# Optimization experiments

Hardware: AMD Instinct MI355X
Metric: run time of the kernel (lower is better)

The kernel has to match this reference:

```python
import jax, jax.numpy as jnp
import numpy as np
from jax import lax

D_MODEL = 1024
D_IN = 1024        # expand=1 -> d_inner = d_model
N_STATE = 16       # d_state
DT_RANK = 64       # ceil(d_model/16)
D_FFN = 4096
BATCH, SEQ = 2, 2048


def setup_inputs() -> dict:
    key = jax.random.key(0)
    ks = jax.random.split(key, 12)
    r = lambda i, shape, s=0.02: jax.random.normal(ks[i], shape, jnp.float32) * s
    ones = lambda n: jnp.ones((n,), jnp.float32)
    zeros = lambda n: jnp.zeros((n,), jnp.float32)
    # S4D-real init for A
    A_log = jnp.log(jnp.tile(jnp.arange(1, N_STATE + 1, dtype=jnp.float32), (D_IN, 1)))
    return {
        "src": jax.random.normal(ks[0], (BATCH, SEQ, D_MODEL), jnp.float32),
        "in_proj_w": r(1, (2 * D_IN, D_MODEL)),
        "conv_w": r(2, (D_IN, 2), 0.5),
        "conv_b": zeros(D_IN),
        "x_proj_w": r(3, (DT_RANK + 2 * N_STATE, D_IN)),
        "dt_proj_w": r(4, (D_IN, DT_RANK), 0.1),
        "dt_proj_b": r(5, (D_IN,), 0.1),
        "A_log": A_log,
        "Dp": ones(D_IN),
        "out_proj_w": r(6, (D_MODEL, D_IN)),
        "mnorm_g": ones(D_MODEL), "mnorm_b": zeros(D_MODEL),
        "n1_g": ones(D_MODEL), "n1_b": zeros(D_MODEL),
        "n2_g": ones(D_MODEL), "n2_b": zeros(D_MODEL),
        "n3_g": ones(D_MODEL), "n3_b": zeros(D_MODEL),
        "ffn_w1": r(7, (D_FFN, D_MODEL)),
        "ffn_w2": r(8, (D_MODEL, D_FFN)),
        "fe_w": r(9, (D_MODEL, D_MODEL)),
        "fe_b": zeros(D_MODEL),
    }


def _ln(x, g, b, eps=1e-5):
    m = x.mean(-1, keepdims=True)
    v = ((x - m) ** 2).mean(-1, keepdims=True)
    return (x - m) / jnp.sqrt(v + eps) * g + b


def _mamba(x, in_proj_w, conv_w, conv_b, x_proj_w, dt_proj_w, dt_proj_b,
           A_log, Dp, out_proj_w):
    B, L, _ = x.shape
    xz = x @ in_proj_w.T                       # (B,L,2*D_IN)
    x_in, z = jnp.split(xz, 2, axis=-1)
    # depthwise causal conv1d, kernel size 2: y[l] = w0*x[l-1] + w1*x[l] + b
    x_prev = jnp.pad(x_in, ((0, 0), (1, 0), (0, 0)))[:, :L]
    x_c = jax.nn.silu(x_prev * conv_w[:, 0] + x_in * conv_w[:, 1] + conv_b)
    x_dbl = x_c @ x_proj_w.T                   # (B,L,DT_RANK+2N)
    dt, Bm, Cm = jnp.split(x_dbl, [DT_RANK, DT_RANK + N_STATE], axis=-1)
    delta = jax.nn.softplus(dt @ dt_proj_w.T + dt_proj_b)   # (B,L,D_IN)
    A = -jnp.exp(A_log)                        # (D_IN,N)
    deltaA = jnp.exp(delta[..., None] * A)                   # (B,L,D_IN,N)
    dBu = delta[..., None] * Bm[:, :, None, :] * x_c[..., None]

    def step(h, t):
        dA_t, dBu_t, C_t = t                   # (B,D_IN,N),(B,D_IN,N),(B,N)
        h = dA_t * h + dBu_t
        y = jnp.einsum('bdn,bn->bd', h, C_t)
        return h, y

    h0 = jnp.zeros((B, D_IN, N_STATE), x.dtype)
    _, ys = lax.scan(step, h0,
                     (deltaA.transpose(1, 0, 2, 3),
                      dBu.transpose(1, 0, 2, 3),
                      Cm.transpose(1, 0, 2)))
    y = ys.transpose(1, 0, 2)                  # (B,L,D_IN)
    y = (y + x_c * Dp) * jax.nn.silu(z)
    return y @ out_proj_w.T


def reference(src, in_proj_w, conv_w, conv_b, x_proj_w, dt_proj_w, dt_proj_b,
              A_log, Dp, out_proj_w, mnorm_g, mnorm_b, n1_g, n1_b, n2_g, n2_b,
              n3_g, n3_b, ffn_w1, ffn_w2, fe_w, fe_b):
    # src1 = MambaBlock(norm1(src)); dropout = identity (eval)
    h = _mamba(_ln(src, n1_g, n1_b), in_proj_w, conv_w, conv_b, x_proj_w,
               dt_proj_w, dt_proj_b, A_log, Dp, out_proj_w)
    src = src + _ln(h, mnorm_g, mnorm_b)
    # FFN: Linear -> LeakyReLU(0.01) -> Linear (no bias)
    f = _ln(src, n2_g, n2_b) @ ffn_w1.T
    f = jnp.where(f >= 0, f, 0.01 * f) @ ffn_w2.T
    src = src + f
    src = src + (_ln(src, n3_g, n3_b) @ fe_w.T + fe_b)
    return src
```

## Files before the change

### kernel.cpp

```cpp
#include <hip/hip_runtime.h>
#include <hip/hip_bf16.h>
#include <cstddef>

#define L_SEQ   2048
#define NBATCH  2
#define NROWS   (NBATCH * L_SEQ)
#define NSTATE  16
#define CH      64
#define NCHUNK  (L_SEQ / CH)

typedef __bf16 bf16x8 __attribute__((ext_vector_type(8)));
typedef float  f32x4  __attribute__((ext_vector_type(4)));
typedef unsigned short u16x4 __attribute__((ext_vector_type(4)));
typedef unsigned short u16x8 __attribute__((ext_vector_type(8)));

static __device__ __forceinline__ unsigned short f2bf(float f) {
  unsigned int x = __builtin_bit_cast(unsigned int, f);
  x += 0x7fffu + ((x >> 16) & 1u);
  return (unsigned short)(x >> 16);
}
static __device__ __forceinline__ float bf2f(unsigned short u) {
  return __builtin_bit_cast(float, ((unsigned int)u) << 16);
}

#define GLDS(g, l) __builtin_amdgcn_global_load_lds( \
    (const __attribute__((address_space(1))) void*)(g), \
    (__attribute__((address_space(3))) void*)(l), 16, 0, 0)

#define DRAIN_VM() asm volatile("s_waitcnt vmcnt(0)" ::: "memory")

__global__ __launch_bounds__(256) void cvt_bf16_kernel(
    const float* __restrict__ in, unsigned short* __restrict__ out, int n4)
{
  const int i = blockIdx.x * 256 + threadIdx.x;
  if (i < n4) {
    const float4 v = reinterpret_cast<const float4*>(in)[i];
    u16x4 o;
    o[0] = f2bf(v.x); o[1] = f2bf(v.y); o[2] = f2bf(v.z); o[3] = f2bf(v.w);
    reinterpret_cast<u16x4*>(out)[i] = o;
  }
}

__global__ __launch_bounds__(256) void cvt_all_kernel(
    const float* __restrict__ ipw, const float* __restrict__ xpw,
    const float* __restrict__ dtw, const float* __restrict__ opw,
    const float* __restrict__ w1,  const float* __restrict__ w2,
    const float* __restrict__ few, float* __restrict__ zx,
    unsigned short* __restrict__ o_ipw, unsigned short* __restrict__ o_xpw,
    unsigned short* __restrict__ o_dtw, unsigned short* __restrict__ o_opw,
    unsigned short* __restrict__ o_w1,  unsigned short* __restrict__ o_w2,
    unsigned short* __restrict__ o_few,
    const float* __restrict__ lsrc, const float* __restrict__ lg,
    const float* __restrict__ lb, unsigned short* __restrict__ louth)
{
  __shared__ float sm[8];
  if (blockIdx.x >= 12832) {
    const int row = blockIdx.x - 12832;
    const int tid = threadIdx.x;
    const float4 v = reinterpret_cast<const float4*>(lsrc + (size_t)row * 1024)[tid];
    float s = v.x + v.y + v.z + v.w;
#pragma unroll
    for (int o = 32; o > 0; o >>= 1) s += __shfl_down(s, o, 64);
    if ((tid & 63) == 0) sm[tid >> 6] = s;
    __syncthreads();
    const float mean = (sm[0] + sm[1] + sm[2] + sm[3]) * (1.f / 1024.f);
    const float dx = v.x - mean, dy = v.y - mean, dz = v.z - mean, dw = v.w - mean;
    float q = dx * dx + dy * dy + dz * dz + dw * dw;
#pragma unroll
    for (int o = 32; o > 0; o >>= 1) q += __shfl_down(q, o, 64);
    __syncthreads();
    if ((tid & 63) == 0) sm[tid >> 6] = q;
    __syncthreads();
    const float var = (sm[0] + sm[1] + sm[2] + sm[3]) * (1.f / 1024.f);
    const float rstd = rsqrtf(var + 1e-5f);
    const float4 gv = reinterpret_cast<const float4*>(lg)[tid];
    const float4 bv = reinterpret_cast<const float4*>(lb)[tid];
    u16x4 ob;
    ob[0] = f2bf(dx * rstd * gv.x + bv.x);
    ob[1] = f2bf(dy * rstd * gv.y + bv.y);
    ob[2] = f2bf(dz * rstd * gv.z + bv.z);
    ob[3] = f2bf(dw * rstd * gv.w + bv.w);
    reinterpret_cast<u16x4*>(louth + (size_t)row * 1024)[tid] = ob;
    return;
  }
  int i = blockIdx.x * 256 + threadIdx.x;
  if (i < 98304) {
    reinterpret_cast<float4*>(zx)[i] = make_float4(0.f, 0.f, 0.f, 0.f);
    return;
  }
  i -= 98304;
  const float* src; unsigned short* dst;
  if (i < 524288)                 { src = ipw; dst = o_ipw; }
  else if ((i -= 524288) < 24576) { src = xpw; dst = o_xpw; }
  else if ((i -= 24576) < 16384)  { src = dtw; dst = o_dtw; }
  else if ((i -= 16384) < 262144) { src = opw; dst = o_opw; }
  else if ((i -= 262144) < 1048576){ src = w1; dst = o_w1; }
  else if ((i -= 1048576) < 1048576){ src = w2; dst = o_w2; }
  else if ((i -= 1048576) < 262144){ src = few; dst = o_few; }
  else return;
  const float4 v = reinterpret_cast<const float4*>(src)[i];
  u16x4 o;
  o[0] = f2bf(v.x); o[1] = f2bf(v.y); o[2] = f2bf(v.z); o[3] = f2bf(v.w);
  reinterpret_cast<u16x4*>(dst)[i] = o;
}

__global__ __launch_bounds__(256) void ln_kernel(
    const float* __restrict__ in, const float* __restrict__ g,
    const float* __restrict__ bta, const float* __restrict__ res,
    float* __restrict__ out, unsigned short* __restrict__ outb)
{
  const int row = blockIdx.x;
  const int tid = threadIdx.x;
  __shared__ float sm[8];
  const float4 v = reinterpret_cast<const float4*>(in + (size_t)row * 1024)[tid];
  float s = v.x + v.y + v.z + v.w;
#pragma unroll
  for (int o = 32; o > 0; o >>= 1) s += __shfl_down(s, o, 64);
  if ((tid & 63) == 0) sm[tid >> 6] = s;
  __syncthreads();
  const float mean = (sm[0] + sm[1] + sm[2] + sm[3]) * (1.f / 1024.f);
  const float dx = v.x - mean, dy = v.y - mean, dz = v.z - mean, dw = v.w - mean;
  float q = dx * dx + dy * dy + dz * dz + dw * dw;
#pragma unroll
  for (int o = 32; o > 0; o >>= 1) q += __shfl_down(q, o, 64);
  __syncthreads();
  if ((tid & 63) == 0) sm[tid >> 6] = q;
  __syncthreads();
  const float var = (sm[0] + sm[1] + sm[2] + sm[3]) * (1.f / 1024.f);
  const float rstd = rsqrtf(var + 1e-5f);
  const float4 gv = reinterpret_cast<const float4*>(g)[tid];
  const float4 bv = reinterpret_cast<const float4*>(bta)[tid];
  float4 o4;
  o4.x = dx * rstd * gv.x + bv.x;
  o4.y = dy * rstd * gv.y + bv.y;
  o4.z = dz * rstd * gv.z + bv.z;
  o4.w = dw * rstd * gv.w + bv.w;
  if (outb) {
    u16x4 ob;
    ob[0] = f2bf(o4.x); ob[1] = f2bf(o4.y); ob[2] = f2bf(o4.z); ob[3] = f2bf(o4.w);
    reinterpret_cast<u16x4*>(outb + (size_t)row * 1024)[tid] = ob;
  } else {
    if (res) {
      const float4 rv = reinterpret_cast<const float4*>(res + (size_t)row * 1024)[tid];
      o4.x += rv.x; o4.y += rv.y; o4.z += rv.z; o4.w += rv.w;
    }
    reinterpret_cast<float4*>(out + (size_t)row * 1024)[tid] = o4;
  }
}

__global__ __launch_bounds__(256) void ln2_kernel(
    const float* __restrict__ in, const float* __restrict__ g1,
    const float* __restrict__ b1, const float* __restrict__ res,
    const float* __restrict__ g2, const float* __restrict__ b2,
    float* __restrict__ out1, unsigned short* __restrict__ out2b)
{
  const int row = blockIdx.x;
  const int tid = threadIdx.x;
  __shared__ float sm[8];
  const float4 v = reinterpret_cast<const float4*>(in + (size_t)row * 1024)[tid];
  float s = v.x + v.y + v.z + v.w;
#pragma unroll
  for (int o = 32; o > 0; o >>= 1) s += __shfl_down(s, o, 64);
  if ((tid & 63) == 0) sm[tid >> 6] = s;
  __syncthreads();
  const float mean = (sm[0] + sm[1] + sm[2] + sm[3]) * (1.f / 1024.f);
  const float dx = v.x - mean, dy = v.y - mean, dz = v.z - mean, dw = v.w - mean;
  float q = dx * dx + dy * dy + dz * dz + dw * dw;
#pragma unroll
  for (int o = 32; o > 0; o >>= 1) q += __shfl_down(q, o, 64);
  __syncthreads();
  if ((tid & 63) == 0) sm[tid >> 6] = q;
  __syncthreads();
  const float var = (sm[0] + sm[1] + sm[2] + sm[3]) * (1.f / 1024.f);
  const float rstd = rsqrtf(var + 1e-5f);
  const float4 g1v = reinterpret_cast<const float4*>(g1)[tid];
  const float4 b1v = reinterpret_cast<const float4*>(b1)[tid];
  const float4 rv = reinterpret_cast<const float4*>(res + (size_t)row * 1024)[tid];
  float4 o4;
  o4.x = dx * rstd * g1v.x + b1v.x + rv.x;
  o4.y = dy * rstd * g1v.y + b1v.y + rv.y;
  o4.z = dz * rstd * g1v.z + b1v.z + rv.z;
  o4.w = dw * rstd * g1v.w + b1v.w + rv.w;
  reinterpret_cast<float4*>(out1 + (size_t)row * 1024)[tid] = o4;
  __syncthreads();
  float s2 = o4.x + o4.y + o4.z + o4.w;
#pragma unroll
  for (int o = 32; o > 0; o >>= 1) s2 += __shfl_down(s2, o, 64);
  if ((tid & 63) == 0) sm[tid >> 6] = s2;
  __syncthreads();
  const float mean2 = (sm[0] + sm[1] + sm[2] + sm[3]) * (1.f / 1024.f);
  const float ex = o4.x - mean2, ey = o4.y - mean2, ez = o4.z - mean2, ew = o4.w - mean2;
  float q2 = ex * ex + ey * ey + ez * ez + ew * ew;
#pragma unroll
  for (int o = 32; o > 0; o >>= 1) q2 += __shfl_down(q2, o, 64);
  __syncthreads();
  if ((tid & 63) == 0) sm[tid >> 6] = q2;
  __syncthreads();
  const float var2 = (sm[0] + sm[1] + sm[2] + sm[3]) * (1.f / 1024.f);
  const float rstd2 = rsqrtf(var2 + 1e-5f);
  const float4 g2v = reinterpret_cast<const float4*>(g2)[tid];
  const float4 b2v = reinterpret_cast<const float4*>(b2)[tid];
  u16x4 ob;
  ob[0] = f2bf(ex * rstd2 * g2v.x + b2v.x);
  ob[1] = f2bf(ey * rstd2 * g2v.y + b2v.y);
  ob[2] = f2bf(ez * rstd2 * g2v.z + b2v.z);
  ob[3] = f2bf(ew * rstd2 * g2v.w + b2v.w);
  reinterpret_cast<u16x4*>(out2b + (size_t)row * 1024)[tid] = ob;
}

__global__ __launch_bounds__(512) void gemm256_kernel(
    const unsigned short* __restrict__ A, int lda,
    const unsigned short* __restrict__ B, int ldb,
    void* __restrict__ Cv, int ldc,
    const float* __restrict__ bias, const float* __restrict__ res,
    int K, int act, int outbf, int gy)
{
  __shared__ __align__(16) unsigned char smem[131072];
  const int t = threadIdx.x;
  const int w = t >> 6, l = t & 63;

  const int q = gridDim.x >> 3;
  const int nid = (blockIdx.x & 7) * q + (blockIdx.x >> 3);
  const int bm = (nid / gy) * 256;
  const int bn = (nid % gy) * 256;

  const int wr = (w >> 2) * 128;
  const int wc = (w & 3) * 64;
  f32x4 acc[8][4] = {};

  const int srow = t >> 2;
  const int sk = (t & 3) * 8;
  const unsigned short* gA = A + (size_t)(bm + srow) * lda + sk;
  const unsigned short* gB = B + (size_t)(bn + srow) * ldb + sk;

  const int fr = l & 15;
  const int kb = (l >> 4) * 8;

#define SA7(s) (smem + (s) * 16384)
#define SB7(s) (smem + 65536 + (s) * 16384)

#define STAGE7(s, k0) do { \
    GLDS(gA + (k0), SA7(s) + w * 1024); \
    GLDS(gA + (k0) + (size_t)128 * lda, SA7(s) + 8192 + w * 1024); \
    GLDS(gB + (k0), SB7(s) + w * 1024); \
    GLDS(gB + (k0) + (size_t)128 * ldb, SB7(s) + 8192 + w * 1024); \
  } while (0)

#define COMPUTE7(s) do { \
    bf16x8 af[8], bfr[4]; \
    _Pragma("unroll") \
    for (int j = 0; j < 4; ++j) \
      bfr[j] = *reinterpret_cast<const bf16x8*>((const unsigned short*)SB7(s) + (wc + j * 16 + fr) * 32 + kb); \
    _Pragma("unroll") \
    for (int i = 0; i < 8; ++i) \
      af[i] = *reinterpret_cast<const bf16x8*>((const unsigned short*)SA7(s) + (wr + i * 16 + fr) * 32 + kb); \
    _Pragma("unroll") \
    for (int i = 0; i < 8; ++i) \
      _Pragma("unroll") \
      for (int j = 0; j < 4; ++j) \
        acc[i][j] = __builtin_amdgcn_mfma_f32_16x16x32_bf16(af[i], bfr[j], acc[i][j], 0, 0, 0); \
  } while (0)

  const int nt = K >> 5;
  STAGE7(0, 0);
  if (nt > 1) STAGE7(1, 32);
  if (nt > 2) STAGE7(2, 64);
  if (nt > 2)      asm volatile("s_waitcnt vmcnt(8)" ::: "memory");
  else if (nt > 1) asm volatile("s_waitcnt vmcnt(4)" ::: "memory");
  else             asm volatile("s_waitcnt vmcnt(0)" ::: "memory");
  __builtin_amdgcn_s_barrier();
  for (int kt = 0; kt < nt; ++kt) {
    const int s = kt & 3;
    __builtin_amdgcn_sched_barrier(0);
    if (kt + 3 < nt) STAGE7((kt + 3) & 3, (kt + 3) * 32);
    __builtin_amdgcn_sched_barrier(0);
    COMPUTE7(s);
    __builtin_amdgcn_sched_barrier(0);
    if (kt + 3 < nt)      asm volatile("s_waitcnt vmcnt(8)" ::: "memory");
    else if (kt + 2 < nt) asm volatile("s_waitcnt vmcnt(4)" ::: "memory");
    else if (kt + 1 < nt) asm volatile("s_waitcnt vmcnt(0)" ::: "memory");
    __builtin_amdgcn_s_barrier();
  }
#undef STAGE7
#undef COMPUTE7
#undef SA7
#undef SB7

  const int crow = (l >> 4) * 4;
  const int ccol = l & 15;
  float* Cf = (float*)Cv;
  unsigned short* Cb = (unsigned short*)Cv;
#pragma unroll
  for (int i = 0; i < 8; ++i) {
#pragma unroll
    for (int j = 0; j < 4; ++j) {
      const int n = bn + wc + j * 16 + ccol;
      const float bv = bias ? bias[n] : 0.f;
#pragma unroll
      for (int r = 0; r < 4; ++r) {
        const int m = bm + wr + i * 16 + crow + r;
        float v = acc[i][j][r] + bv;
        if (act == 1) v = (v > 20.f) ? v : __logf(1.f + __expf(v));
        else if (act == 2) v = (v >= 0.f) ? v : 0.01f * v;
        if (res) v += res[(size_t)m * ldc + n];
        if (outbf) Cb[(size_t)m * ldc + n] = f2bf(v);
        else       Cf[(size_t)m * ldc + n] = v;
      }
    }
  }
}

template<int BK>
__global__ __launch_bounds__(512) void gemm_ksplit_kernel(
    const unsigned short* __restrict__ A, int lda,
    const unsigned short* __restrict__ B, int ldb,
    void* __restrict__ Cv, int ldc,
    const float* __restrict__ bias, const float* __restrict__ res,
    int K, int act, int outbf, int gy)
{
  constexpr int ABYTES = 128 * BK * 2;
  constexpr int NISS = (BK == 32) ? 2 : 4;
  constexpr int RPI  = (BK == 32) ? 64 : 32;
  constexpr int NS   = BK / 32;
  __shared__ __align__(16) unsigned char smem[8 * ABYTES];
  const int tid = threadIdx.x;
  const int grp = tid >> 8;
  const int t = tid & 255;
  const int w = t >> 6, l = t & 63;

  const int q = gridDim.x >> 3;
  const int nid = (blockIdx.x & 7) * q + (blockIdx.x >> 3);
  const int bm = (nid / gy) * 128;
  const int bn = (nid % gy) * 128;

  const int K2 = K >> 1;
  const int koff = grp * K2;
  const int wr = (w >> 1) * 64, wc = (w & 1) * 64;
  f32x4 acc[4][4] = {};

  const int srow = (BK == 32) ? (t >> 2) : (t >> 3);
  const int sk   = (BK == 32) ? ((t & 3) * 8) : ((t & 7) * 8);
  const unsigned short* gA = A + (size_t)(bm + srow) * lda + koff + sk;
  const unsigned short* gB = B + (size_t)(bn + srow) * ldb + koff + sk;

  const int gbase = grp * 2 * ABYTES;
  const int fr = l & 15;
  const int kb = (l >> 4) * 8;

#define SAb(buf) (smem + gbase + (buf) * ABYTES)
#define SBb(buf) (smem + 4 * ABYTES + gbase + (buf) * ABYTES)

#define STAGEK(buf, k0) do { \
    _Pragma("unroll") \
    for (int ii = 0; ii < NISS; ++ii) { \
      GLDS(gA + (k0) + (size_t)ii * RPI * lda, SAb(buf) + ii * 4096 + w * 1024); \
      GLDS(gB + (k0) + (size_t)ii * RPI * ldb, SBb(buf) + ii * 4096 + w * 1024); \
    } \
  } while (0)

#define COMPUTEK(buf) do { \
    _Pragma("unroll") \
    for (int s = 0; s < NS; ++s) { \
      bf16x8 af[4], bfr[4]; \
      _Pragma("unroll") \
      for (int i = 0; i < 4; ++i) \
        af[i] = *reinterpret_cast<const bf16x8*>((const unsigned short*)SAb(buf) + (wr + i * 16 + fr) * BK + s * 32 + kb); \
      _Pragma("unroll") \
      for (int j = 0; j < 4; ++j) \
        bfr[j] = *reinterpret_cast<const bf16x8*>((const unsigned short*)SBb(buf) + (wc + j * 16 + fr) * BK + s * 32 + kb); \
      _Pragma("unroll") \
      for (int i = 0; i < 4; ++i) \
        _Pragma("unroll") \
        for (int j = 0; j < 4; ++j) \
          acc[i][j] = __builtin_amdgcn_mfma_f32_16x16x32_bf16(af[i], bfr[j], acc[i][j], 0, 0, 0); \
    } \
  } while (0)

  STAGEK(0, 0);
  DRAIN_VM();
  __syncthreads();
  int cur = 0;
  for (int k0 = BK; k0 < K2; k0 += BK) {
    __builtin_amdgcn_sched_barrier(0);
    STAGEK(cur ^ 1, k0);
    __builtin_amdgcn_sched_barrier(0);
    COMPUTEK(cur);
    DRAIN_VM();
    __syncthreads();
    cur ^= 1;
  }
  COMPUTEK(cur);
#undef STAGEK
#undef COMPUTEK
#undef SAb
#undef SBb

  __syncthreads();
  float* red = (float*)smem;
  if (grp) {
#pragma unroll
    for (int i = 0; i < 4; ++i)
#pragma unroll
      for (int j = 0; j < 4; ++j)
        *reinterpret_cast<f32x4*>(&red[(t << 6) + (i * 4 + j) * 4]) = acc[i][j];
  }
  __syncthreads();
  if (!grp) {
    const int crow = (l >> 4) * 4;
    const int ccol = l & 15;
    float* Cf = (float*)Cv;
    unsigned short* Cb = (unsigned short*)Cv;
#pragma unroll
    for (int i = 0; i < 4; ++i) {
#pragma unroll
      for (int j = 0; j < 4; ++j) {
        const f32x4 o = *reinterpret_cast<const f32x4*>(&red[(t << 6) + (i * 4 + j) * 4]);
        const int n = bn + wc + j * 16 + ccol;
        const float bv = bias ? bias[n] : 0.f;
#pragma unroll
        for (int r = 0; r < 4; ++r) {
          const int m = bm + wr + i * 16 + crow + r;
          float v = acc[i][j][r] + o[r] + bv;
          if (act == 1) v = (v > 20.f) ? v : __logf(1.f + __expf(v));
          else if (act == 2) v = (v >= 0.f) ? v : 0.01f * v;
          if (res) v += res[(size_t)m * ldc + n];
          if (outbf) Cb[(size_t)m * ldc + n] = f2bf(v);
          else       Cf[(size_t)m * ldc + n] = v;
        }
      }
    }
  }
}

__global__ __launch_bounds__(256) void xproj_kernel(
    const unsigned short* __restrict__ A, int lda,
    const unsigned short* __restrict__ B, int ldb,
    float* __restrict__ C)
{
  __shared__ unsigned short As[2][128 * 32];
  __shared__ unsigned short Bs[2][96 * 32];
  const int t = threadIdx.x;
  const int w = t >> 6, l = t & 63;
  const int bm = blockIdx.x * 128;
  const int kbase = blockIdx.y * 128;

  f32x4 acc[2][6] = {};

  const int srow = t >> 2;
  const int sk = (t & 3) * 8;
  const unsigned short* gA0 = A + (size_t)(bm + srow) * lda + kbase + sk;
  const unsigned short* gA1 = gA0 + (size_t)64 * lda;
  const unsigned short* gB0 = B + (size_t)srow * ldb + kbase + sk;
  const unsigned short* gB1 = gB0 + (size_t)64 * ldb;

  const int fr = l & 15;
  const int kb = (l >> 4) * 8;

#define STAGEX(buf, k0) do { \
    GLDS(gA0 + (k0), &As[buf][w * 512]); \
    GLDS(gA1 + (k0), &As[buf][2048 + w * 512]); \
    GLDS(gB0 + (k0), &Bs[buf][w * 512]); \
    if (w < 2) GLDS(gB1 + (k0), &Bs[buf][2048 + w * 512]); \
  } while (0)

#define COMPUTEX(buf) do { \
    bf16x8 af[2], bfr[6]; \
    _Pragma("unroll") \
    for (int i = 0; i < 2; ++i) \
      af[i] = *reinterpret_cast<const bf16x8*>(&As[buf][(w * 32 + i * 16 + fr) * 32 + kb]); \
    _Pragma("unroll") \
    for (int j = 0; j < 6; ++j) \
      bfr[j] = *reinterpret_cast<const bf16x8*>(&Bs[buf][(j * 16 + fr) * 32 + kb]); \
    _Pragma("unroll") \
    for (int i = 0; i < 2; ++i) \
      _Pragma("unroll") \
      for (int j = 0; j < 6; ++j) \
        acc[i][j] = __builtin_amdgcn_mfma_f32_16x16x32_bf16(af[i], bfr[j], acc[i][j], 0, 0, 0); \
  } while (0)

  STAGEX(0, 0);
  DRAIN_VM();
  __syncthreads();
  int cur = 0;
  for (int s = 1; s < 4; ++s) {
    __builtin_amdgcn_sched_barrier(0);
    STAGEX(cur ^ 1, s * 32);
    __builtin_amdgcn_sched_barrier(0);
    COMPUTEX(cur);
    DRAIN_VM();
    __syncthreads();
    cur ^= 1;
  }
  COMPUTEX(cur);
#undef STAGEX
#undef COMPUTEX

  const int crow = (l >> 4) * 4;
  const int ccol = l & 15;
#pragma unroll
  for (int i = 0; i < 2; ++i)
#pragma unroll
    for (int j = 0; j < 6; ++j)
#pragma unroll
      for (int r = 0; r < 4; ++r) {
        const int m = bm + w * 32 + i * 16 + crow + r;
        const int n = j * 16 + ccol;
        atomicAdd(&C[(size_t)m * 96 + n], acc[i][j][r]);
      }
}

__global__ __launch_bounds__(256) void conv_silu_kernel(
    const unsigned short* __restrict__ xz, const float* __restrict__ cw,
    const float* __restrict__ cb, unsigned short* __restrict__ xcb)
{
  const int i = blockIdx.x * 256 + threadIdx.x;
  const int row = i >> 7;
  const int dv = (i & 127) * 8;
  const int l = row & (L_SEQ - 1);
  const u16x8 cur = *reinterpret_cast<const u16x8*>(&xz[(size_t)row * 2048 + dv]);
  u16x8 prev = {};
  if (l != 0) prev = *reinterpret_cast<const u16x8*>(&xz[(size_t)(row - 1) * 2048 + dv]);
  float cwv[16], cbv[8];
#pragma unroll
  for (int qq = 0; qq < 4; ++qq)
    *reinterpret_cast<float4*>(&cwv[qq * 4]) = reinterpret_cast<const float4*>(cw + 2 * dv)[qq];
#pragma unroll
  for (int qq = 0; qq < 2; ++qq)
    *reinterpret_cast<float4*>(&cbv[qq * 4]) = reinterpret_cast<const float4*>(cb + dv)[qq];
  u16x8 o;
#pragma unroll
  for (int e = 0; e < 8; ++e) {
    const float v = bf2f(prev[e]) * cwv[2 * e] + bf2f(cur[e]) * cwv[2 * e + 1] + cbv[e];
    o[e] = f2bf(v / (1.f + __expf(-v)));
  }
  *reinterpret_cast<u16x8*>(&xcb[(size_t)row * 1024 + dv]) = o;
}

__global__ __launch_bounds__(256) void scan_pass1(
    const unsigned short* __restrict__ delta, const unsigned short* __restrict__ xc,
    const float* __restrict__ xdbl, const float* __restrict__ A_log,
    unsigned short* __restrict__ hfin, unsigned short* __restrict__ pcum)
{
  const int tid = threadIdx.x;
  const int db = blockIdx.x & 3;
  const int c = (blockIdx.x >> 2) & (NCHUNK - 1);
  const int b = blockIdx.x >> 7;
  const int d = db * 256 + tid;
  __shared__ float Bsh[CH][16];
  {
    const int lr = tid >> 2, q = tid & 3;
    const float* p = xdbl + ((size_t)(b * L_SEQ + c * CH + lr) * 96) + 64 + q * 4;
    *reinterpret_cast<float4*>(&Bsh[lr][q * 4]) = *reinterpret_cast<const float4*>(p);
  }
  float a[NSTATE];
#pragma unroll
  for (int n = 0; n < NSTATE; ++n) a[n] = -__expf(A_log[d * 16 + n]);
  __syncthreads();
  float h[NSTATE], P[NSTATE];
#pragma unroll
  for (int n = 0; n < NSTATE; ++n) { h[n] = 0.f; P[n] = 1.f; }
  const size_t rowbase = (size_t)(b * L_SEQ + c * CH);
  for (int s = 0; s < CH; ++s) {
    const size_t row = rowbase + s;
    const float dl = bf2f(delta[row * 1024 + d]);
    const float xcv = bf2f(xc[row * 1024 + d]);
#pragma unroll
    for (int n = 0; n < NSTATE; ++n) {
      const float dA = __expf(dl * a[n]);
      h[n] = h[n] * dA + (dl * Bsh[s][n]) * xcv;
      P[n] *= dA;
    }
  }
  const size_t base = ((size_t)((b * NCHUNK + c) * 1024 + d)) * 16;
  u16x8 h0, h1, p0, p1;
#pragma unroll
  for (int n = 0; n < 8; ++n) {
    h0[n] = f2bf(h[n]);     h1[n] = f2bf(h[n + 8]);
    p0[n] = f2bf(P[n]);     p1[n] = f2bf(P[n + 8]);
  }
  *reinterpret_cast<u16x8*>(hfin + base) = h0;
  *reinterpret_cast<u16x8*>(hfin + base + 8) = h1;
  *reinterpret_cast<u16x8*>(pcum + base) = p0;
  *reinterpret_cast<u16x8*>(pcum + base + 8) = p1;
}

__global__ __launch_bounds__(256) void scan_pass2(
    const unsigned short* __restrict__ hfin, const unsigned short* __restrict__ pcum,
    unsigned short* __restrict__ hstart)
{
  const int t = blockIdx.x * 256 + threadIdx.x;
  const int b = t >> 14;
  const int dn = t & 16383;
  const size_t base = (size_t)b * NCHUNK * 16384 + dn;
  float h = 0.f;
  for (int c = 0; c < NCHUNK; ++c) {
    const size_t idx = base + (size_t)c * 16384;
    hstart[idx] = f2bf(h);
    h = bf2f(pcum[idx]) * h + bf2f(hfin[idx]);
  }
}

__global__ __launch_bounds__(256) void scan_pass3(
    const unsigned short* __restrict__ delta, const unsigned short* __restrict__ xc,
    const float* __restrict__ xdbl, const float* __restrict__ A_log,
    const unsigned short* __restrict__ hstart, const float* __restrict__ Dp,
    const unsigned short* __restrict__ xz, unsigned short* __restrict__ yout)
{
  const int tid = threadIdx.x;
  const int db = blockIdx.x & 3;
  const int c = (blockIdx.x >> 2) & (NCHUNK - 1);
  const int b = blockIdx.x >> 7;
  const int d = db * 256 + tid;
  __shared__ float Bsh[CH][16];
  __shared__ float Csh[CH][16];
  {
    const int lr = tid >> 2, q = tid & 3;
    const float* p = xdbl + ((size_t)(b * L_SEQ + c * CH + lr) * 96);
    *reinterpret_cast<float4*>(&Bsh[lr][q * 4]) = *reinterpret_cast<const float4*>(p + 64 + q * 4);
    *reinterpret_cast<float4*>(&Csh[lr][q * 4]) = *reinterpret_cast<const float4*>(p + 80 + q * 4);
  }
  float a[NSTATE];
#pragma unroll
  for (int n = 0; n < NSTATE; ++n) a[n] = -__expf(A_log[d * 16 + n]);
  float h[NSTATE];
  {
    const size_t base = ((size_t)((b * NCHUNK + c) * 1024 + d)) * 16;
    const u16x8 v0 = *reinterpret_cast<const u16x8*>(hstart + base);
    const u16x8 v1 = *reinterpret_cast<const u16x8*>(hstart + base + 8);
#pragma unroll
    for (int n = 0; n < 8; ++n) { h[n] = bf2f(v0[n]); h[n + 8] = bf2f(v1[n]); }
  }
  const float dpv = Dp[d];
  __syncthreads();
  const size_t rowbase = (size_t)(b * L_SEQ + c * CH);
  for (int s = 0; s < CH; ++s) {
    const size_t row = rowbase + s;
    const float dl = bf2f(delta[row * 1024 + d]);
    const float xcv = bf2f(xc[row * 1024 + d]);
    float y = 0.f;
#pragma unroll
    for (int n = 0; n < NSTATE; ++n) {
      const float dA = __expf(dl * a[n]);
      h[n] = h[n] * dA + (dl * Bsh[s][n]) * xcv;
      y += h[n] * Csh[s][n];
    }
    const float z = bf2f(xz[row * 2048 + 1024 + d]);
    const float sil = z / (1.f + __expf(-z));
    yout[row * 1024 + d] = f2bf((y + xcv * dpv) * sil);
  }
}

extern "C" void kernel_launch(void* const* d_in, const int* in_sizes, int n_in,
                              void* d_out, int out_size, void* d_ws, size_t ws_size,
                              hipStream_t stream)
{
  (void)in_sizes; (void)n_in; (void)out_size; (void)ws_size;
  const float* src        = (const float*)d_in[0];
  const float* in_proj_w  = (const float*)d_in[1];
  const float* conv_w     = (const float*)d_in[2];
  const float* conv_b     = (const float*)d_in[3];
  const float* x_proj_w   = (const float*)d_in[4];
  const float* dt_proj_w  = (const float*)d_in[5];
  const float* dt_proj_b  = (const float*)d_in[6];
  const float* A_log      = (const float*)d_in[7];
  const float* Dp         = (const float*)d_in[8];
  const float* out_proj_w = (const float*)d_in[9];
  const float* mnorm_g    = (const float*)d_in[10];
  const float* mnorm_b    = (const float*)d_in[11];
  const float* n1_g       = (const float*)d_in[12];
  const float* n1_b       = (const float*)d_in[13];
  const float* n2_g       = (const float*)d_in[14];
  const float* n2_b       = (const float*)d_in[15];
  const float* n3_g       = (const float*)d_in[16];
  const float* n3_b       = (const float*)d_in[17];
  const float* ffn_w1     = (const float*)d_in[18];
  const float* ffn_w2     = (const float*)d_in[19];
  const float* fe_w       = (const float*)d_in[20];
  const float* fe_b       = (const float*)d_in[21];
  float* out = (float*)d_out;
  float* ws  = (float*)d_ws;

  unsigned short* xzb   = (unsigned short*)ws;
  unsigned short* xdblb = (unsigned short*)(ws + 4194304);
  unsigned short* dtwb  = (unsigned short*)(ws + 4390912);
  unsigned short* deltab= (unsigned short*)(ws + 4423680);
  float* xdbl  = ws + 12582912;
  float* s5    = ws + 17301504;
  float* src1  = ws + 21495808;
  unsigned short* hfin = (unsigned short*)(ws + 25690112);
  unsigned short* pcum = (unsigned short*)(ws + 26738688);
  unsigned short* hst  = (unsigned short*)(ws + 27787264);
  unsigned short* s1b  = (unsigned short*)(ws + 28835840);
  unsigned short* xcb  = (unsigned short*)(ws + 30932992);
  unsigned short* yb   = (unsigned short*)(ws + 33030144);
  unsigned short* f1b  = (unsigned short*)(ws + 35127296);
  unsigned short* ipwb = (unsigned short*)(ws + 43515904);
  unsigned short* xpwb = (unsigned short*)(ws + 44564480);
  unsigned short* opwb = (unsigned short*)(ws + 44613632);
  unsigned short* w1b  = (unsigned short*)(ws + 45137920);
  unsigned short* w2b  = (unsigned short*)(ws + 47235072);
  unsigned short* fewb = (unsigned short*)(ws + 49332224);

  const dim3 blk(256);
  const dim3 blk512(512);

  cvt_all_kernel<<<16928, blk, 0, stream>>>(
      in_proj_w, x_proj_w, dt_proj_w, out_proj_w, ffn_w1, ffn_w2, fe_w, xdbl,
      ipwb, xpwb, dtwb, opwb, w1b, w2b, fewb,
      src, n1_g, n1_b, s1b);

  gemm_ksplit_kernel<32><<<512, blk512, 0, stream>>>(s1b, 1024, ipwb, 1024, xzb, 2048,
                                                     nullptr, nullptr, 1024, 0, 1, 16);
  conv_silu_kernel<<<2048, blk, 0, stream>>>(xzb, conv_w, conv_b, xcb);
  xproj_kernel<<<dim3(32, 8), blk, 0, stream>>>(xcb, 1024, xpwb, 1024, xdbl);
  cvt_bf16_kernel<<<384, blk, 0, stream>>>(xdbl, xdblb, 98304);
  gemm_ksplit_kernel<32><<<256, blk512, 0, stream>>>(xdblb, 96, dtwb, 64, deltab, 1024,
                                                     dt_proj_b, nullptr, 64, 1, 1, 8);
  scan_pass1<<<256, blk, 0, stream>>>(deltab, xcb, xdbl, A_log, hfin, pcum);
  scan_pass2<<<128, blk, 0, stream>>>(hfin, pcum, hst);
  scan_pass3<<<256, blk, 0, stream>>>(deltab, xcb, xdbl, A_log, hst, Dp, xzb, yb);
  gemm_ksplit_kernel<64><<<256, blk512, 0, stream>>>(yb, 1024, opwb, 1024, s5, 1024,
                                                     nullptr, nullptr, 1024, 0, 0, 8);
  ln2_kernel<<<NROWS, blk, 0, stream>>>(s5, mnorm_g, mnorm_b, src,
                                        n2_g, n2_b, src1, s1b);
  gemm256_kernel<<<256, blk512, 0, stream>>>(s1b, 1024, w1b, 1024, f1b, 4096,
                                             nullptr, nullptr, 1024, 2, 1, 16);
  gemm_ksplit_kernel<64><<<256, blk512, 0, stream>>>(f1b, 4096, w2b, 4096, s5, 1024,
                                                     nullptr, src1, 4096, 0, 0, 8);
  ln_kernel<<<NROWS, blk, 0, stream>>>(s5, n3_g, n3_b, nullptr, nullptr, s1b);
  gemm_ksplit_kernel<64><<<256, blk512, 0, stream>>>(s1b, 1024, fewb, 1024, out, 1024,
                                                     fe_b, s5, 1024, 0, 0, 8);
}
```

Baseline: 375.7 us.

## Add four-stage ring-buffered k-split GEMM for output, FFN2 and final projections

Adds a new k-split GEMM kernel that keeps a four-slot shared-memory ring with BK=32, issuing loads three tiles ahead and waiting with partial vmcnt counts instead of fully draining each iteration. The three 128x128 output GEMMs (out_proj, FFN second layer, final linear) switch to it from the double-buffered BK=64 kernel. The goal is to hide global-load latency behind MFMA work. In exchange it uses 128 KB of LDS per block, which may limit occupancy, and its hand-written wait counts are fragile.

```diff
diff --git a/kernel.cpp b/kernel.cpp
--- a/kernel.cpp
+++ b/kernel.cpp
@@ -394,6 +394,124 @@
 #undef COMPUTEK
 #undef SAb
 #undef SBb
+
+  __syncthreads();
+  float* red = (float*)smem;
+  if (grp) {
+#pragma unroll
+    for (int i = 0; i < 4; ++i)
+#pragma unroll
+      for (int j = 0; j < 4; ++j)
+        *reinterpret_cast<f32x4*>(&red[(t << 6) + (i * 4 + j) * 4]) = acc[i][j];
+  }
+  __syncthreads();
+  if (!grp) {
+    const int crow = (l >> 4) * 4;
+    const int ccol = l & 15;
+    float* Cf = (float*)Cv;
+    unsigned short* Cb = (unsigned short*)Cv;
+#pragma unroll
+    for (int i = 0; i < 4; ++i) {
+#pragma unroll
+      for (int j = 0; j < 4; ++j) {
+        const f32x4 o = *reinterpret_cast<const f32x4*>(&red[(t << 6) + (i * 4 + j) * 4]);
+        const int n = bn + wc + j * 16 + ccol;
+        const float bv = bias ? bias[n] : 0.f;
+#pragma unroll
+        for (int r = 0; r < 4; ++r) {
+          const int m = bm + wr + i * 16 + crow + r;
+          float v = acc[i][j][r] + o[r] + bv;
+          if (act == 1) v = (v > 20.f) ? v : __logf(1.f + __expf(v));
+          else if (act == 2) v = (v >= 0.f) ? v : 0.01f * v;
+          if (res) v += res[(size_t)m * ldc + n];
+          if (outbf) Cb[(size_t)m * ldc + n] = f2bf(v);
+          else       Cf[(size_t)m * ldc + n] = v;
+        }
+      }
+    }
+  }
+}
+
+__global__ __launch_bounds__(512) void gemm_ksplit_ring_kernel(
+    const unsigned short* __restrict__ A, int lda,
+    const unsigned short* __restrict__ B, int ldb,
+    void* __restrict__ Cv, int ldc,
+    const float* __restrict__ bias, const float* __restrict__ res,
+    int K, int act, int outbf, int gy)
+{
+  __shared__ __align__(16) unsigned char smem[131072];
+  const int tid = threadIdx.x;
+  const int grp = tid >> 8;
+  const int t = tid & 255;
+  const int w = t >> 6, l = t & 63;
+
+  const int q = gridDim.x >> 3;
+  const int nid = (blockIdx.x & 7) * q + (blockIdx.x >> 3);
+  const int bm = (nid / gy) * 128;
+  const int bn = (nid % gy) * 128;
+
+  const int K2 = K >> 1;
+  const int koff = grp * K2;
+  const int wr = (w >> 1) * 64, wc = (w & 1) * 64;
+  f32x4 acc[4][4] = {};
+
+  const int srow = t >> 2;
+  const int sk = (t & 3) * 8;
+  const unsigned short* gA = A + (size_t)(bm + srow) * lda + koff + sk;
+  const unsigned short* gB = B + (size_t)(bn + srow) * ldb + koff + sk;
+
+  const int fr = l & 15;
+  const int kb = (l >> 4) * 8;
+
+#define SAr(s) (smem + grp * 32768 + (s) * 8192)
+#define SBr(s) (smem + 65536 + grp * 32768 + (s) * 8192)
+
+#define STAGER(s, k0) do { \
+    GLDS(gA + (k0), SAr(s) + w * 1024); \
+    GLDS(gA + (k0) + (size_t)64 * lda, SAr(s) + 4096 + w * 1024); \
+    GLDS(gB + (k0), SBr(s) + w * 1024); \
+    GLDS(gB + (k0) + (size_t)64 * ldb, SBr(s) + 4096 + w * 1024); \
+  } while (0)
+
+#define COMPUTER(s) do { \
+    bf16x8 af[4], bfr[4]; \
+    _Pragma("unroll") \
+    for (int i = 0; i < 4; ++i) \
+      af[i] = *reinterpret_cast<const bf16x8*>((const unsigned short*)SAr(s) + (wr + i * 16 + fr) * 32 + kb); \
+    _Pragma("unroll") \
+    for (int j = 0; j < 4; ++j) \
+      bfr[j] = *reinterpret_cast<const bf16x8*>((const unsigned short*)SBr(s) + (wc + j * 16 + fr) * 32 + kb); \
+    _Pragma("unroll") \
+    for (int i = 0; i < 4; ++i) \
+      _Pragma("unroll") \
+      for (int j = 0; j < 4; ++j) \
+        acc[i][j] = __builtin_amdgcn_mfma_f32_16x16x32_bf16(af[i], bfr[j], acc[i][j], 0, 0, 0); \
+  } while (0)
+
+  const int nt = K2 >> 5;
+  STAGER(0, 0);
+  if (nt > 1) STAGER(1, 32);
+  if (nt > 2) STAGER(2, 64);
+  if (nt > 2)      asm volatile("s_waitcnt vmcnt(8)" ::: "memory");
+  else if (nt > 1) asm volatile("s_waitcnt vmcnt(4)" ::: "memory");
+  else             asm volatile("s_waitcnt vmcnt(0)" ::: "memory");
+  __builtin_amdgcn_s_barrier();
+  for (int kt = 0; kt < nt; ++kt) {
+    const int s = kt & 3;
+    __builtin_amdgcn_sched_barrier(0);
+    if (kt + 3 < nt) STAGER((kt + 3) & 3, (kt + 3) * 32);
+    __builtin_amdgcn_sched_barrier(0);
+    COMPUTER(s);
+    __builtin_amdgcn_sched_barrier(0);
+    if (kt + 3 < nt)      asm volatile("s_waitcnt vmcnt(8)" ::: "memory");
+    else if (kt + 2 < nt) asm volatile("s_waitcnt vmcnt(4)" ::: "memory");
+    else if (kt + 1 < nt) asm volatile("s_waitcnt vmcnt(0)" ::: "memory");
+    __builtin_amdgcn_s_barrier();
+  }
+#undef STAGER
+#undef COMPUTER
+#undef SAr
+#undef SBr
 
   __syncthreads();
   float* red = (float*)smem;
@@ -719,15 +837,15 @@
   scan_pass1<<<256, blk, 0, stream>>>(deltab, xcb, xdbl, A_log, hfin, pcum);
   scan_pass2<<<128, blk, 0, stream>>>(hfin, pcum, hst);
   scan_pass3<<<256, blk, 0, stream>>>(deltab, xcb, xdbl, A_log, hst, Dp, xzb, yb);
-  gemm_ksplit_kernel<64><<<256, blk512, 0, stream>>>(yb, 1024, opwb, 1024, s5, 1024,
-                                                     nullptr, nullptr, 1024, 0, 0, 8);
+  gemm_ksplit_ring_kernel<<<256, blk512, 0, stream>>>(yb, 1024, opwb, 1024, s5, 1024,
+                                                      nullptr, nullptr, 1024, 0, 0, 8);
   ln2_kernel<<<NROWS, blk, 0, stream>>>(s5, mnorm_g, mnorm_b, src,
                                         n2_g, n2_b, src1, s1b);
   gemm256_kernel<<<256, blk512, 0, stream>>>(s1b, 1024, w1b, 1024, f1b, 4096,
                                              nullptr, nullptr, 1024, 2, 1, 16);
-  gemm_ksplit_kernel<64><<<256, blk512, 0, stream>>>(f1b, 4096, w2b, 4096, s5, 1024,
-                                                     nullptr, src1, 4096, 0, 0, 8);
+  gemm_ksplit_ring_kernel<<<256, blk512, 0, stream>>>(f1b, 4096, w2b, 4096, s5, 1024,
+                                                      nullptr, src1, 4096, 0, 0, 8);
   ln_kernel<<<NROWS, blk, 0, stream>>>(s5, n3_g, n3_b, nullptr, nullptr, s1b);
-  gemm_ksplit_kernel<64><<<256, blk512, 0, stream>>>(s1b, 1024, fewb, 1024, out, 1024,
-                                                     fe_b, s5, 1024, 0, 0, 8);
-}
+  gemm_ksplit_ring_kernel<<<256, blk512, 0, stream>>>(s1b, 1024, fewb, 1024, out, 1024,
+                                                      fe_b, s5, 1024, 0, 0, 8);
+}
```

Result: no change. 375.1 us, median of 2 (-0.2%).
